# Optimization experiments

Hardware: AMD Instinct MI355X
Metric: run time of the kernel (lower is better)

The kernel has to match this reference:

```python
import jax, jax.numpy as jnp
import numpy as np
import math

HAD = 1024  # hadamard_size hard-coded in HiggsLinear

def _hadamard_matrix(n):
    H = np.array([[1.0]], dtype=np.float32)
    while H.shape[0] < n:
        H = np.block([[H, H], [H, -H]])
    return H

# normalized Hadamard (scale = 1/sqrt(1024)); symmetric, so x @ _H == H x per block
_H = jnp.asarray(_hadamard_matrix(HAD) / math.sqrt(HAD))

def setup_inputs() -> dict:
    key = jax.random.key(0)
    k1, k2, k3, k4, k5 = jax.random.split(key, 5)
    in_f, out_f, d, n_codes, tokens = 4096, 4096, 2, 256, 8192
    return {
        "x": jax.random.normal(k1, (tokens, in_f), jnp.float32),
        "codes": jax.random.randint(k2, (out_f, in_f // d), 0, n_codes, jnp.int32),
        "grid": jax.random.normal(k3, (n_codes, d), jnp.float32),
        "scales": jax.random.uniform(k4, (out_f, in_f // HAD), jnp.float32, 0.5, 1.5),
        "bias": jax.random.normal(k5, (out_f,), jnp.float32),
    }

def reference(x, codes, grid, scales, bias):
    d = grid.shape[1]
    out_f = codes.shape[0]
    post = ((HAD - 1) // d + 1) * d  # post_hadamard_size
    # --- dequantize weight: codebook gather + per-hadamard-group scale ---
    W = grid[codes]                               # (out, num_higgs_groups, d)
    W = W.reshape(out_f, -1, post)[..., :HAD]     # (out, n_had_groups, 1024)
    W = W * scales[..., None]
    W = W.reshape(out_f, -1)                      # (out, in)
    # --- blockwise Hadamard transform of input (block = 1024) ---
    nh = x.shape[-1] // HAD
    xh = x.reshape(x.shape[:-1] + (nh, HAD)) @ _H
    xh = xh.reshape(x.shape[:-1] + (nh * HAD,))
    # --- fused dequant matmul equivalent: F.linear(xh, W, bias) ---
    return xh @ W.T + bias
```

## Files before the change

### kernel.cpp

```cpp
#include <hip/hip_runtime.h>

#define M_TOK 8192
#define N_OUT 4096
#define K_IN  4096
#define NT    (K_IN / 64)
#define CVT_BLOCKS ((M_TOK * K_IN) / 2048)
#define DEQ_BLOCKS (N_OUT * 4 / 4)

typedef __bf16 bf16x8 __attribute__((ext_vector_type(8)));
typedef float f32x4 __attribute__((ext_vector_type(4)));

__device__ __forceinline__ unsigned short f2b(float f) {
  union { float f; unsigned u; } c; c.f = f;
  unsigned u = c.u;
  return (unsigned short)((u + 0x7FFFu + ((u >> 16) & 1u)) >> 16);
}

__global__ __launch_bounds__(256) void prep_kernel(const float* __restrict__ x,
                                                   unsigned short* __restrict__ xb,
                                                   const int* __restrict__ codes,
                                                   const float* __restrict__ grid,
                                                   const float* __restrict__ scales,
                                                   unsigned short* __restrict__ Wt) {
  if (blockIdx.x < CVT_BLOCKS) {
    long i = ((long)blockIdx.x * 256 + threadIdx.x) * 8;
    float4 a = *(const float4*)(x + i);
    float4 b = *(const float4*)(x + i + 4);
    union { unsigned short us[8]; uint4 v; } o;
    o.us[0] = f2b(a.x); o.us[1] = f2b(a.y); o.us[2] = f2b(a.z); o.us[3] = f2b(a.w);
    o.us[4] = f2b(b.x); o.us[5] = f2b(b.y); o.us[6] = f2b(b.z); o.us[7] = f2b(b.w);
    *(uint4*)(xb + i) = o.v;
  } else {
    int bid = blockIdx.x - CVT_BLOCKS;
    int wave = threadIdx.x >> 6;
    int lane = threadIdx.x & 63;
    int G = bid * 4 + wave;
    int o = G >> 2;
    int g = G & 3;
    const int* crow = codes + (long)o * 2048 + g * 512 + lane * 8;
    int4 c0 = *(const int4*)crow;
    int4 c1 = *(const int4*)(crow + 4);
    float v[16];
    const float2* g2p = (const float2*)grid;
    float2 t;
    t = g2p[c0.x]; v[0] = t.x;  v[1] = t.y;
    t = g2p[c0.y]; v[2] = t.x;  v[3] = t.y;
    t = g2p[c0.z]; v[4] = t.x;  v[5] = t.y;
    t = g2p[c0.w]; v[6] = t.x;  v[7] = t.y;
    t = g2p[c1.x]; v[8] = t.x;  v[9] = t.y;
    t = g2p[c1.y]; v[10] = t.x; v[11] = t.y;
    t = g2p[c1.z]; v[12] = t.x; v[13] = t.y;
    t = g2p[c1.w]; v[14] = t.x; v[15] = t.y;
#pragma unroll
    for (int s = 1; s < 16; s <<= 1) {
#pragma unroll
      for (int base = 0; base < 16; base++) {
        if (!(base & s)) {
          float a = v[base], b = v[base | s];
          v[base] = a + b;
          v[base | s] = a - b;
        }
      }
    }
#pragma unroll
    for (int m = 1; m <= 32; m <<= 1) {
      bool hi = (lane & m) != 0;
#pragma unroll
      for (int c = 0; c < 16; c++) {
        float p = __shfl_xor(v[c], m, 64);
        v[c] = hi ? p - v[c] : p + v[c];
      }
    }
    float sc = scales[o * 4 + g] * 0.03125f;
    union { unsigned short us[16]; uint4 q[2]; } out;
#pragma unroll
    for (int c = 0; c < 16; c++) out.us[c] = f2b(v[c] * sc);
    unsigned short* wp = Wt + (long)o * 4096 + g * 1024 + lane * 16;
    *(uint4*)wp = out.q[0];
    *(uint4*)(wp + 8) = out.q[1];
  }
}

__device__ __forceinline__ void load16_to_lds(const unsigned short* g, unsigned short* l) {
  __builtin_amdgcn_global_load_lds((const __attribute__((address_space(1))) void*)g,
                                   (__attribute__((address_space(3))) void*)l,
                                   16, 0, 0);
}

__device__ __forceinline__ void phase_barrier() {
  __builtin_amdgcn_s_barrier();
  __builtin_amdgcn_sched_barrier(0);
}

__global__ __launch_bounds__(512, 2) void gemm_kernel(const unsigned short* __restrict__ A,
                                                      const unsigned short* __restrict__ B,
                                                      const float* __restrict__ bias,
                                                      float* __restrict__ C) {
  __shared__ unsigned short sA[2][256 * 64];
  __shared__ unsigned short sB[2][256 * 64];

  const int wg  = blockIdx.x;
  const int swz = (wg & 7) * (512 / 8) + (wg >> 3);
  const int bn  = (swz & 15) * 256;
  const int bm  = (swz >> 4) * 256;

  const int tid  = threadIdx.x;
  const int wave = tid >> 6;
  const int lane = tid & 63;
  const int wm   = wave >> 2;
  const int wn   = wave & 3;

  const long K = K_IN;
  const unsigned short* aSrc[4];
  const unsigned short* bSrc[4];
  unsigned short* aDst[4];
  unsigned short* bDst[4];
#pragma unroll
  for (int j = 0; j < 4; j++) {
    const int g   = tid + j * 512;
    const int row = g >> 3;
    const int cg  = (g & 7) ^ (row & 7);
    aSrc[j] = A + (long)(bm + row) * K + cg * 8;
    bSrc[j] = B + (long)(bn + row) * K + cg * 8;
    aDst[j] = &sA[0][g * 8];
    bDst[j] = &sB[0][g * 8];
  }

  const int m7  = lane & 7;
  const int cb  = lane >> 4;
  const int r0a = wm * 128 + (lane & 15);
  const int r0b = wn * 64  + (lane & 15);
  const int aoff0 = (r0a * 8 + ( cb      ^ m7)) * 8;
  const int aoff1 = (r0a * 8 + ((cb | 4) ^ m7)) * 8;
  const int boff0 = (r0b * 8 + ( cb      ^ m7)) * 8;
  const int boff1 = (r0b * 8 + ((cb | 4) ^ m7)) * 8;

  f32x4 acc[8][4] = {};

#pragma unroll
  for (int j = 0; j < 4; j++) {
    load16_to_lds(aSrc[j], aDst[j]);
    load16_to_lds(bSrc[j], bDst[j]);
  }

  for (int t = 0; t < NT; t++) {
    const int p = t & 1;
    const unsigned short* bufA = &sA[p][0];
    const unsigned short* bufB = &sB[p][0];

    if (t + 1 < NT) {
      const int koff = (t + 1) * 64;
      const int q16  = ((t + 1) & 1) * 16384;
#pragma unroll
      for (int j = 0; j < 4; j++) {
        load16_to_lds(aSrc[j] + koff, aDst[j] + q16);
        load16_to_lds(bSrc[j] + koff, bDst[j] + q16);
      }
      asm volatile("s_waitcnt vmcnt(8)" ::: "memory");
    } else {
      asm volatile("s_waitcnt vmcnt(0)" ::: "memory");
    }
    phase_barrier();

    bf16x8 a0[4], a1[4], b0[4];

#pragma unroll
    for (int i = 0; i < 4; i++) b0[i] = *(const bf16x8*)(bufB + boff0 + i * 1024);
#pragma unroll
    for (int i = 0; i < 4; i++) a0[i] = *(const bf16x8*)(bufA + aoff0 + i * 1024);
    phase_barrier();
    __builtin_amdgcn_s_setprio(1);
#pragma unroll
    for (int mi = 0; mi < 4; mi++)
#pragma unroll
      for (int ni = 0; ni < 4; ni++)
        acc[mi][ni] = __builtin_amdgcn_mfma_f32_16x16x32_bf16(a0[mi], b0[ni], acc[mi][ni], 0, 0, 0);
    __builtin_amdgcn_s_setprio(0);
    phase_barrier();

#pragma unroll
    for (int i = 0; i < 4; i++) a1[i] = *(const bf16x8*)(bufA + aoff0 + 4096 + i * 1024);
    phase_barrier();
    __builtin_amdgcn_s_setprio(1);
#pragma unroll
    for (int mi = 0; mi < 4; mi++)
#pragma unroll
      for (int ni = 0; ni < 4; ni++)
        acc[4 + mi][ni] = __builtin_amdgcn_mfma_f32_16x16x32_bf16(a1[mi], b0[ni], acc[4 + mi][ni], 0, 0, 0);
    __builtin_amdgcn_s_setprio(0);
    phase_barrier();

#pragma unroll
    for (int i = 0; i < 4; i++) b0[i] = *(const bf16x8*)(bufB + boff1 + i * 1024);
#pragma unroll
    for (int i = 0; i < 4; i++) a0[i] = *(const bf16x8*)(bufA + aoff1 + i * 1024);
    phase_barrier();
    __builtin_amdgcn_s_setprio(1);
#pragma unroll
    for (int mi = 0; mi < 4; mi++)
#pragma unroll
      for (int ni = 0; ni < 4; ni++)
        acc[mi][ni] = __builtin_amdgcn_mfma_f32_16x16x32_bf16(a0[mi], b0[ni], acc[mi][ni], 0, 0, 0);
    __builtin_amdgcn_s_setprio(0);
    phase_barrier();

#pragma unroll
    for (int i = 0; i < 4; i++) a1[i] = *(const bf16x8*)(bufA + aoff1 + 4096 + i * 1024);
    phase_barrier();
    __builtin_amdgcn_s_setprio(1);
#pragma unroll
    for (int mi = 0; mi < 4; mi++)
#pragma unroll
      for (int ni = 0; ni < 4; ni++)
        acc[4 + mi][ni] = __builtin_amdgcn_mfma_f32_16x16x32_bf16(a1[mi], b0[ni], acc[4 + mi][ni], 0, 0, 0);
    __builtin_amdgcn_s_setprio(0);
    phase_barrier();
  }

  const int cn  = lane & 15;
  const int cm4 = (lane >> 4) * 4;
#pragma unroll
  for (int ni = 0; ni < 4; ni++) {
    const int col = bn + wn * 64 + ni * 16 + cn;
    const float bb = bias[col];
#pragma unroll
    for (int mi = 0; mi < 8; mi++) {
#pragma unroll
      for (int r = 0; r < 4; r++) {
        const int row = bm + wm * 128 + mi * 16 + cm4 + r;
        C[(long)row * N_OUT + col] = acc[mi][ni][r] + bb;
      }
    }
  }
}

extern "C" void kernel_launch(void* const* d_in, const int* in_sizes, int n_in,
                              void* d_out, int out_size, void* d_ws, size_t ws_size,
                              hipStream_t stream) {
  const float* x      = (const float*)d_in[0];
  const int*   codes  = (const int*)d_in[1];
  const float* grid   = (const float*)d_in[2];
  const float* scales = (const float*)d_in[3];
  const float* bias   = (const float*)d_in[4];
  float* out = (float*)d_out;

  unsigned short* xb = (unsigned short*)d_ws;
  unsigned short* Wt = xb + (size_t)M_TOK * K_IN;

  prep_kernel<<<CVT_BLOCKS + DEQ_BLOCKS, 256, 0, stream>>>(x, xb, codes, grid, scales, Wt);
  gemm_kernel<<<512, 512, 0, stream>>>(xb, Wt, bias, out);
}
```

Baseline: 585.0 us.

## Interleave next-tile global-to-LDS prefetch across MFMA phases with partial waits

The eight global_load_lds copies for the next K tile were issued in one burst at the top of each iteration. They are now split into four pairs, each placed inside one of the four LDS-read/MFMA phases. The vmcnt waits are relaxed so that the A rows needed only by the second half of the tile can still be in flight while the first MFMAs run. This is meant to spread memory traffic across the iteration and hide load latency behind compute. In exchange it depends on exact vmcnt counting and on the row-to-load mapping, which makes the schedule more fragile.

```diff
diff --git a/kernel.cpp b/kernel.cpp
--- a/kernel.cpp
+++ b/kernel.cpp
@@ -137,30 +137,24 @@
 
   f32x4 acc[8][4] = {};
 
-#pragma unroll
-  for (int j = 0; j < 4; j++) {
-    load16_to_lds(aSrc[j], aDst[j]);
-    load16_to_lds(bSrc[j], bDst[j]);
-  }
+  load16_to_lds(bSrc[0], bDst[0]);
+  load16_to_lds(bSrc[1], bDst[1]);
+  load16_to_lds(bSrc[2], bDst[2]);
+  load16_to_lds(bSrc[3], bDst[3]);
+  load16_to_lds(aSrc[0], aDst[0]);
+  load16_to_lds(aSrc[2], aDst[2]);
+  load16_to_lds(aSrc[1], aDst[1]);
+  load16_to_lds(aSrc[3], aDst[3]);
+  asm volatile("s_waitcnt vmcnt(2)" ::: "memory");
+  phase_barrier();
 
   for (int t = 0; t < NT; t++) {
     const int p = t & 1;
     const unsigned short* bufA = &sA[p][0];
     const unsigned short* bufB = &sB[p][0];
-
-    if (t + 1 < NT) {
-      const int koff = (t + 1) * 64;
-      const int q16  = ((t + 1) & 1) * 16384;
-#pragma unroll
-      for (int j = 0; j < 4; j++) {
-        load16_to_lds(aSrc[j] + koff, aDst[j] + q16);
-        load16_to_lds(bSrc[j] + koff, bDst[j] + q16);
-      }
-      asm volatile("s_waitcnt vmcnt(8)" ::: "memory");
-    } else {
-      asm volatile("s_waitcnt vmcnt(0)" ::: "memory");
-    }
-    phase_barrier();
+    const bool pf   = (t + 1 < NT);
+    const int  koff = (t + 1) * 64;
+    const int  q16  = (p ^ 1) * 16384;
 
     bf16x8 a0[4], a1[4], b0[4];
 
@@ -168,6 +162,10 @@
     for (int i = 0; i < 4; i++) b0[i] = *(const bf16x8*)(bufB + boff0 + i * 1024);
 #pragma unroll
     for (int i = 0; i < 4; i++) a0[i] = *(const bf16x8*)(bufA + aoff0 + i * 1024);
+    if (pf) {
+      load16_to_lds(bSrc[0] + koff, bDst[0] + q16);
+      load16_to_lds(bSrc[1] + koff, bDst[1] + q16);
+    }
     phase_barrier();
     __builtin_amdgcn_s_setprio(1);
 #pragma unroll
@@ -176,10 +174,16 @@
       for (int ni = 0; ni < 4; ni++)
         acc[mi][ni] = __builtin_amdgcn_mfma_f32_16x16x32_bf16(a0[mi], b0[ni], acc[mi][ni], 0, 0, 0);
     __builtin_amdgcn_s_setprio(0);
+    if (pf) asm volatile("s_waitcnt vmcnt(2)" ::: "memory");
+    else    asm volatile("s_waitcnt vmcnt(0)" ::: "memory");
     phase_barrier();
 
 #pragma unroll
     for (int i = 0; i < 4; i++) a1[i] = *(const bf16x8*)(bufA + aoff0 + 4096 + i * 1024);
+    if (pf) {
+      load16_to_lds(bSrc[2] + koff, bDst[2] + q16);
+      load16_to_lds(bSrc[3] + koff, bDst[3] + q16);
+    }
     phase_barrier();
     __builtin_amdgcn_s_setprio(1);
 #pragma unroll
@@ -194,6 +198,10 @@
     for (int i = 0; i < 4; i++) b0[i] = *(const bf16x8*)(bufB + boff1 + i * 1024);
 #pragma unroll
     for (int i = 0; i < 4; i++) a0[i] = *(const bf16x8*)(bufA + aoff1 + i * 1024);
+    if (pf) {
+      load16_to_lds(aSrc[0] + koff, aDst[0] + q16);
+      load16_to_lds(aSrc[2] + koff, aDst[2] + q16);
+    }
     phase_barrier();
     __builtin_amdgcn_s_setprio(1);
 #pragma unroll
@@ -206,6 +214,10 @@
 
 #pragma unroll
     for (int i = 0; i < 4; i++) a1[i] = *(const bf16x8*)(bufA + aoff1 + 4096 + i * 1024);
+    if (pf) {
+      load16_to_lds(aSrc[1] + koff, aDst[1] + q16);
+      load16_to_lds(aSrc[3] + koff, aDst[3] + q16);
+    }
     phase_barrier();
     __builtin_amdgcn_s_setprio(1);
 #pragma unroll
@@ -214,6 +226,7 @@
       for (int ni = 0; ni < 4; ni++)
         acc[4 + mi][ni] = __builtin_amdgcn_mfma_f32_16x16x32_bf16(a1[mi], b0[ni], acc[4 + mi][ni], 0, 0, 0);
     __builtin_amdgcn_s_setprio(0);
+    if (pf) asm volatile("s_waitcnt vmcnt(2)" ::: "memory");
     phase_barrier();
   }
 
```

New measurement: 546.6 us. 1.07x faster.
